# Performance work log

Measured on AMD Instinct MI355X. Metric: run time of the kernel, lower is better.

## Reference

```python
import jax, jax.numpy as jnp
import numpy as np

B, N, C = 2, 4096, 1024
H, WIN = 16, 20
D = C // H

def setup_inputs() -> dict:
    key = jax.random.key(0)
    ks = jax.random.split(key, 9)
    s = 1.0 / np.sqrt(C)
    d = {"q": jax.random.normal(ks[0], (B, N, C), jnp.float32)}
    for i, name in enumerate(["Wq", "Wk", "Wv", "Wo"]):
        d[name + "_w"] = jax.random.normal(ks[1 + 2 * i], (C, C), jnp.float32) * s
        d[name + "_b"] = jax.random.normal(ks[2 + 2 * i], (C,), jnp.float32) * 0.01
    return d

def reference(q, Wq_w, Wq_b, Wk_w, Wk_b, Wv_w, Wv_b, Wo_w, Wo_b):
    b, n, c = q.shape
    w2 = WIN // 2  # half window = 10
    def proj(x, w, bias):
        return (x @ w.T + bias).reshape(b, n, H, D).transpose(0, 2, 1, 3)  # [B,H,N,D]
    Q = proj(q, Wq_w, Wq_b)
    K = proj(q, Wk_w, Wk_b)
    V = proj(q, Wv_w, Wv_b)
    off = jnp.arange(-w2, w2 + 1)                       # [Wn] = 21 offsets
    pos = jnp.arange(n)[:, None] + off[None, :]         # [N, Wn] key index per query
    valid = (pos >= 0) & (pos < n)                      # edge clipping == torch start/end slicing
    idx = jnp.clip(pos, 0, n - 1)
    Kw = K[:, :, idx, :]                                # [B,H,N,Wn,D] gathered key windows
    Vw = V[:, :, idx, :]
    scale = jnp.sqrt(jnp.float32(D))
    scores = jnp.einsum('bhnd,bhnwd->bhnw', Q, Kw) / scale
    scores = jnp.where(valid[None, None], scores, -jnp.inf)
    probs = jax.nn.softmax(scores, axis=-1)             # invalid slots get exactly 0
    out = jnp.einsum('bhnw,bhnwd->bhnd', probs, Vw)
    out = out.transpose(0, 2, 1, 3).reshape(b, n, c)
    out = out @ Wo_w.T + Wo_b
    # torch returns attn_probs of the LAST loop iteration i=N-1: window [N-1-w2, N), size w2+1
    attn_last = probs[:, :, -1:, : w2 + 1]              # [B,H,1,11]
    return (out, attn_last)
```

## Files before the change

### kernel.cpp

```cpp
#include <hip/hip_runtime.h>
#include <hip/hip_bf16.h>

#define Bb 2
#define Nn 4096
#define Cc 1024
#define Hh 16
#define Dd 64
#define Mm (Bb*Nn)
#define W2 10
#define WINSZ 21

typedef __attribute__((ext_vector_type(8))) short  bf16x8s;
typedef __attribute__((ext_vector_type(4))) float  f32x4;
typedef __attribute__((ext_vector_type(4))) unsigned short us4;

#define AS1 __attribute__((address_space(1)))
#define AS3 __attribute__((address_space(3)))

__device__ __forceinline__ unsigned short f2bf(float f) {
  unsigned int u = __float_as_uint(f);
  u += 0x7FFFu + ((u >> 16) & 1u);
  return (unsigned short)(u >> 16);
}
__device__ __forceinline__ float bflo(unsigned int u) { return __uint_as_float(u << 16); }
__device__ __forceinline__ float bfhi(unsigned int u) { return __uint_as_float(u & 0xFFFF0000u); }

__global__ __launch_bounds__(256) void f2bf_kernel(const float4* __restrict__ src,
                                                   us4* __restrict__ dst, int n4) {
  int stride = gridDim.x * 256;
  for (int i = blockIdx.x * 256 + threadIdx.x; i < n4; i += stride) {
    float4 v = src[i];
    us4 o;
    o.x = f2bf(v.x); o.y = f2bf(v.y); o.z = f2bf(v.z); o.w = f2bf(v.w);
    dst[i] = o;
  }
}

template<bool OUT_BF16>
__global__ __launch_bounds__(512) void gemm_p3(const unsigned short* __restrict__ A,
                                               const unsigned short* __restrict__ Bm,
                                               const float* __restrict__ bias,
                                               void* __restrict__ Cout,
                                               int N) {
  constexpr int K = 1024, NT = 16;
  __shared__ unsigned short lds[3][24576];

  const int tid = threadIdx.x, wid = tid >> 6, lane = tid & 63;
  const int wm = wid >> 2, wn = wid & 3;

  const int nwg = gridDim.x, cpx = nwg >> 3, bid = blockIdx.x;
  const int swz = (bid & 7) * cpx + (bid >> 3);
  const int nbn = N >> 8;
  const int m0 = (swz / nbn) << 7, n0 = (swz % nbn) << 8;

  const int rbase = wid * 8 + (lane >> 3);
  const int cst = ((lane & 7) ^ (lane >> 3)) * 8;
  const unsigned short* aS0 = A + (size_t)(m0 + rbase) * K + cst;
  const unsigned short* aS1 = A + (size_t)(m0 + 64 + rbase) * K + cst;
  const unsigned short* bS0 = Bm + (size_t)(n0 + rbase) * K + cst;
  const unsigned short* bS1 = Bm + (size_t)(n0 + 64 + rbase) * K + cst;
  const unsigned short* bS2 = Bm + (size_t)(n0 + 128 + rbase) * K + cst;
  const unsigned short* bS3 = Bm + (size_t)(n0 + 192 + rbase) * K + cst;
  const int dA0 = wid * 512, dA1 = 4096 + wid * 512;
  const int dB0 = 8192 + wid * 512, dB1 = 12288 + wid * 512;
  const int dB2 = 16384 + wid * 512, dB3 = 20480 + wid * 512;

#define STG(bf, kt) do {                                                                   \
    const size_t ko = (size_t)(kt) * 64;                                                   \
    __builtin_amdgcn_global_load_lds((AS1 const void*)(aS0 + ko), (AS3 void*)(&lds[bf][dA0]), 16, 0, 0); \
    __builtin_amdgcn_global_load_lds((AS1 const void*)(aS1 + ko), (AS3 void*)(&lds[bf][dA1]), 16, 0, 0); \
    __builtin_amdgcn_global_load_lds((AS1 const void*)(bS0 + ko), (AS3 void*)(&lds[bf][dB0]), 16, 0, 0); \
    __builtin_amdgcn_global_load_lds((AS1 const void*)(bS1 + ko), (AS3 void*)(&lds[bf][dB1]), 16, 0, 0); \
    __builtin_amdgcn_global_load_lds((AS1 const void*)(bS2 + ko), (AS3 void*)(&lds[bf][dB2]), 16, 0, 0); \
    __builtin_amdgcn_global_load_lds((AS1 const void*)(bS3 + ko), (AS3 void*)(&lds[bf][dB3]), 16, 0, 0); \
  } while (0)

  int aoff[2][4], boff[2][4];
#pragma unroll
  for (int kk = 0; kk < 2; ++kk) {
    const int chs = ((kk * 4 + (lane >> 4)) ^ (lane & 7)) * 8;
#pragma unroll
    for (int f = 0; f < 4; ++f) {
      aoff[kk][f] = (wm * 64 + f * 16 + (lane & 15)) * 64 + chs;
      boff[kk][f] = 8192 + (wn * 64 + f * 16 + (lane & 15)) * 64 + chs;
    }
  }

  f32x4 acc[4][4] = {};

  STG(0, 0);
  STG(1, 1);
  asm volatile("s_waitcnt vmcnt(6)" ::: "memory");
  __builtin_amdgcn_sched_barrier(0);
  __builtin_amdgcn_s_barrier();
  __builtin_amdgcn_sched_barrier(0);

  int cur = 0, stg = 2;
  for (int t = 0; t < NT; ++t) {
    if (t + 2 < NT) STG(stg, t + 2);

    const unsigned short* L = &lds[cur][0];
    bf16x8s a[2][4], b[2][4];
#pragma unroll
    for (int kk = 0; kk < 2; ++kk) {
#pragma unroll
      for (int f = 0; f < 4; ++f) {
        a[kk][f] = *(const bf16x8s*)(L + aoff[kk][f]);
        b[kk][f] = *(const bf16x8s*)(L + boff[kk][f]);
      }
    }
    __builtin_amdgcn_s_setprio(1);
#pragma unroll
    for (int kk = 0; kk < 2; ++kk)
#pragma unroll
      for (int fm = 0; fm < 4; ++fm)
#pragma unroll
        for (int fn = 0; fn < 4; ++fn)
          acc[fm][fn] = __builtin_amdgcn_mfma_f32_16x16x32_bf16(a[kk][fm], b[kk][fn], acc[fm][fn], 0, 0, 0);
    __builtin_amdgcn_s_setprio(0);

    if (t + 1 < NT) {
      if (t + 2 < NT) asm volatile("s_waitcnt vmcnt(6)" ::: "memory");
      else            asm volatile("s_waitcnt vmcnt(0)" ::: "memory");
      __builtin_amdgcn_sched_barrier(0);
      __builtin_amdgcn_s_barrier();
      __builtin_amdgcn_sched_barrier(0);
    }
    cur = (cur == 2) ? 0 : cur + 1;
    stg = (stg == 2) ? 0 : stg + 1;
  }
#undef STG

  const int r0 = m0 + wm * 64 + (lane >> 4) * 4;
  const int c0 = n0 + wn * 64 + (lane & 15);
#pragma unroll
  for (int fm = 0; fm < 4; ++fm) {
#pragma unroll
    for (int fn = 0; fn < 4; ++fn) {
      const int col = c0 + fn * 16;
      const float bv = bias[col];
#pragma unroll
      for (int r = 0; r < 4; ++r) {
        const int row = r0 + fm * 16 + r;
        const float v = acc[fm][fn][r] + bv;
        if (OUT_BF16)
          ((unsigned short*)Cout)[(size_t)row * N + col] = f2bf(v);
        else
          ((float*)Cout)[(size_t)row * N + col] = v;
      }
    }
  }
}

#define TN 128
#define KVROWS (TN + 2 * W2)

__global__ void attn_kernel(const unsigned short* __restrict__ QKV,
                            unsigned short* __restrict__ AO,
                            float* __restrict__ attn_last) {
  __shared__ uint4 Kl[KVROWS * 8];
  __shared__ uint4 Vl[KVROWS * 8];

  const int nt = Nn / TN;
  const int bid = blockIdx.x;
  const int tile = bid & (nt - 1);
  const int bh = bid / nt;
  const int h = bh & (Hh - 1), b = bh / Hh;
  const int n0 = tile * TN;
  const int tid = threadIdx.x;

  for (int idx = tid; idx < KVROWS * 8; idx += 256) {
    const int r = idx >> 3, c = idx & 7;
    const int pos = n0 - W2 + r;
    uint4 kv = make_uint4(0, 0, 0, 0), vv = make_uint4(0, 0, 0, 0);
    if (pos >= 0 && pos < Nn) {
      const uint4* row = (const uint4*)(QKV + (size_t)(b * Nn + pos) * 3072);
      kv = row[128 + h * 8 + c];
      vv = row[256 + h * 8 + c];
    }
    const int slot = c ^ (r & 7);
    Kl[r * 8 + slot] = kv;
    Vl[r * 8 + slot] = vv;
  }
  __syncthreads();

  const int row  = tid >> 1;
  const int half = tid & 1;
  const int n = n0 + row;
  const size_t m = (size_t)b * Nn + n;

  const uint4* qrow = (const uint4*)(QKV + m * 3072) + h * 8 + half * 4;
  const uint4 qd0 = qrow[0], qd1 = qrow[1], qd2 = qrow[2], qd3 = qrow[3];

  float p[WINSZ];
#pragma unroll
  for (int w = 0; w < WINSZ; ++w) p[w] = 0.f;

#pragma unroll
  for (int c = 0; c < 4; ++c) {
    const uint4 qv = (c == 0) ? qd0 : (c == 1) ? qd1 : (c == 2) ? qd2 : qd3;
    const float q0 = bflo(qv.x), q1 = bfhi(qv.x);
    const float q2 = bflo(qv.y), q3 = bfhi(qv.y);
    const float q4 = bflo(qv.z), q5 = bfhi(qv.z);
    const float q6 = bflo(qv.w), q7 = bfhi(qv.w);
#pragma unroll 7
    for (int w = 0; w < WINSZ; ++w) {
      const int r = row + w;
      const uint4 v = Kl[r * 8 + ((half * 4 + c) ^ (r & 7))];
      float a0 = q0 * bflo(v.x);
      float a1 = q1 * bfhi(v.x);
      a0 += q2 * bflo(v.y);
      a1 += q3 * bfhi(v.y);
      a0 += q4 * bflo(v.z);
      a1 += q5 * bfhi(v.z);
      a0 += q6 * bflo(v.w);
      a1 += q7 * bfhi(v.w);
      p[w] += a0 + a1;
    }
  }

#pragma unroll
  for (int w = 0; w < WINSZ; ++w) {
    float t = p[w];
    t += __shfl_xor(t, 1, 64);
    const int pos = n - W2 + w;
    p[w] = (pos < 0 || pos >= Nn) ? -1e30f : t * 0.125f;
  }
  float mx = p[0];
#pragma unroll
  for (int w = 1; w < WINSZ; ++w) mx = fmaxf(mx, p[w]);
  float sum = 0.f;
#pragma unroll
  for (int w = 0; w < WINSZ; ++w) { p[w] = __expf(p[w] - mx); sum += p[w]; }
  const float inv = 1.0f / sum;

  if (n == Nn - 1 && half == 0) {
#pragma unroll
    for (int w = 0; w <= W2; ++w)
      attn_last[(b * Hh + h) * (W2 + 1) + w] = p[w] * inv;
  }

  uint4* orow = (uint4*)(AO + m * Cc + h * Dd) + half * 4;
#pragma unroll
  for (int c = 0; c < 4; ++c) {
    float o0 = 0.f, o1 = 0.f, o2 = 0.f, o3 = 0.f;
    float o4 = 0.f, o5 = 0.f, o6 = 0.f, o7 = 0.f;
#pragma unroll 7
    for (int w = 0; w < WINSZ; ++w) {
      const int r = row + w;
      const uint4 v = Vl[r * 8 + ((half * 4 + c) ^ (r & 7))];
      const float pw = p[w];
      o0 += pw * bflo(v.x);
      o1 += pw * bfhi(v.x);
      o2 += pw * bflo(v.y);
      o3 += pw * bfhi(v.y);
      o4 += pw * bflo(v.z);
      o5 += pw * bfhi(v.z);
      o6 += pw * bflo(v.w);
      o7 += pw * bfhi(v.w);
    }
    unsigned int d0 = (unsigned int)f2bf(o0 * inv) | ((unsigned int)f2bf(o1 * inv) << 16);
    unsigned int d1 = (unsigned int)f2bf(o2 * inv) | ((unsigned int)f2bf(o3 * inv) << 16);
    unsigned int d2 = (unsigned int)f2bf(o4 * inv) | ((unsigned int)f2bf(o5 * inv) << 16);
    unsigned int d3 = (unsigned int)f2bf(o6 * inv) | ((unsigned int)f2bf(o7 * inv) << 16);
    orow[c] = make_uint4(d0, d1, d2, d3);
  }
}

extern "C" void kernel_launch(void* const* d_in, const int* in_sizes, int n_in,
                              void* d_out, int out_size, void* d_ws, size_t ws_size,
                              hipStream_t stream) {
  const float* q    = (const float*)d_in[0];
  const float* Wq_w = (const float*)d_in[1];
  const float* Wq_b = (const float*)d_in[2];
  const float* Wk_w = (const float*)d_in[3];
  const float* Wk_b = (const float*)d_in[4];
  const float* Wv_w = (const float*)d_in[5];
  const float* Wv_b = (const float*)d_in[6];
  const float* Wo_w = (const float*)d_in[7];
  const float* Wo_b = (const float*)d_in[8];
  float* out = (float*)d_out;
  float* attn_last = out + (size_t)Mm * Cc;

  char* ws = (char*)d_ws;
  unsigned short* qb   = (unsigned short*)(ws);
  unsigned short* Wqkv = (unsigned short*)(ws + 16777216);
  unsigned short* Wo16 = (unsigned short*)(ws + 16777216 + 6291456);
  float*          bqkv = (float*)(ws + 25165824);
  unsigned short* QKV  = (unsigned short*)(ws + 25182208);
  unsigned short* AO   = (unsigned short*)(ws + 75513856);

  {
    int n4 = (Mm * Cc) / 4;
    f2bf_kernel<<<2048, 256, 0, stream>>>((const float4*)q, (us4*)qb, n4);
    int w4 = (Cc * Cc) / 4;
    f2bf_kernel<<<1024, 256, 0, stream>>>((const float4*)Wq_w, (us4*)(Wqkv), w4);
    f2bf_kernel<<<1024, 256, 0, stream>>>((const float4*)Wk_w, (us4*)(Wqkv + Cc * Cc), w4);
    f2bf_kernel<<<1024, 256, 0, stream>>>((const float4*)Wv_w, (us4*)(Wqkv + 2 * Cc * Cc), w4);
    f2bf_kernel<<<1024, 256, 0, stream>>>((const float4*)Wo_w, (us4*)Wo16, w4);
    hipMemcpyAsync(bqkv,          Wq_b, Cc * sizeof(float), hipMemcpyDeviceToDevice, stream);
    hipMemcpyAsync(bqkv + Cc,     Wk_b, Cc * sizeof(float), hipMemcpyDeviceToDevice, stream);
    hipMemcpyAsync(bqkv + 2 * Cc, Wv_b, Cc * sizeof(float), hipMemcpyDeviceToDevice, stream);
  }

  {
    dim3 grid((Mm / 128) * (3072 / 256));
    gemm_p3<true><<<grid, 512, 0, stream>>>(qb, Wqkv, bqkv, (void*)QKV, 3072);
  }

  {
    dim3 grid(Bb * Hh * (Nn / TN));
    attn_kernel<<<grid, 256, 0, stream>>>(QKV, AO, attn_last);
  }

  {
    dim3 grid((Mm / 128) * (Cc / 256));
    gemm_p3<false><<<grid, 512, 0, stream>>>(AO, Wo16, Wo_b, (void*)out, Cc);
  }
}
```

Baseline: 150.7 us.

## Fuse conversion kernels into one launch and switch GEMM to K=32 tiles

Five separate fp32-to-bf16 conversion launches and three bias memcpys are merged into a single grid-stride kernel, which removes launch and memcpy overhead. Separately, the GEMM k-tile shrinks from 64 to 32. That halves LDS use per stage, drops the XOR swizzle, and doubles the number of main-loop iterations and barriers. The unswizzled LDS layout may cause bank conflicts, and the extra barriers add synchronization cost.

New measurement: 145.9 us. -3.2%, faster.

```diff
diff --git a/kernel.cpp b/kernel.cpp
--- a/kernel.cpp
+++ b/kernel.cpp
@@ -25,25 +25,53 @@
 __device__ __forceinline__ float bflo(unsigned int u) { return __uint_as_float(u << 16); }
 __device__ __forceinline__ float bfhi(unsigned int u) { return __uint_as_float(u & 0xFFFF0000u); }
 
-__global__ __launch_bounds__(256) void f2bf_kernel(const float4* __restrict__ src,
-                                                   us4* __restrict__ dst, int n4) {
-  int stride = gridDim.x * 256;
-  for (int i = blockIdx.x * 256 + threadIdx.x; i < n4; i += stride) {
-    float4 v = src[i];
-    us4 o;
-    o.x = f2bf(v.x); o.y = f2bf(v.y); o.z = f2bf(v.z); o.w = f2bf(v.w);
-    dst[i] = o;
+__device__ __forceinline__ us4 cvt4(float4 v) {
+  us4 o;
+  o.x = f2bf(v.x); o.y = f2bf(v.y); o.z = f2bf(v.z); o.w = f2bf(v.w);
+  return o;
+}
+
+__global__ __launch_bounds__(256) void cvt_all(const float4* __restrict__ q,
+                                               const float4* __restrict__ wq,
+                                               const float4* __restrict__ wk,
+                                               const float4* __restrict__ wv,
+                                               const float4* __restrict__ wo,
+                                               const float* __restrict__ bq,
+                                               const float* __restrict__ bk,
+                                               const float* __restrict__ bv,
+                                               us4* __restrict__ qb4,
+                                               us4* __restrict__ wqkv4,
+                                               us4* __restrict__ wo4,
+                                               float* __restrict__ bqkv) {
+  const int NQ = 2097152, NW = 262144, TOT = NQ + 4 * NW;
+  const int gid = blockIdx.x * 256 + threadIdx.x;
+  const int stride = gridDim.x * 256;
+  for (int i = gid; i < TOT; i += stride) {
+    if (i < NQ) {
+      qb4[i] = cvt4(q[i]);
+    } else {
+      int j = i - NQ;
+      int r = j >> 18, k = j & (NW - 1);
+      if (r == 0)      wqkv4[k]          = cvt4(wq[k]);
+      else if (r == 1) wqkv4[NW + k]     = cvt4(wk[k]);
+      else if (r == 2) wqkv4[2 * NW + k] = cvt4(wv[k]);
+      else             wo4[k]            = cvt4(wo[k]);
+    }
+  }
+  if (gid < 3072) {
+    float v = (gid < 1024) ? bq[gid] : (gid < 2048) ? bk[gid - 1024] : bv[gid - 2048];
+    bqkv[gid] = v;
   }
 }
 
 template<bool OUT_BF16>
-__global__ __launch_bounds__(512) void gemm_p3(const unsigned short* __restrict__ A,
-                                               const unsigned short* __restrict__ Bm,
-                                               const float* __restrict__ bias,
-                                               void* __restrict__ Cout,
-                                               int N) {
-  constexpr int K = 1024, NT = 16;
-  __shared__ unsigned short lds[3][24576];
+__global__ __launch_bounds__(512) void gemm_k32(const unsigned short* __restrict__ A,
+                                                const unsigned short* __restrict__ Bm,
+                                                const float* __restrict__ bias,
+                                                void* __restrict__ Cout,
+                                                int N) {
+  constexpr int K = 1024, NT = 32;
+  __shared__ unsigned short lds[3][12288];
 
   const int tid = threadIdx.x, wid = tid >> 6, lane = tid & 63;
   const int wm = wid >> 2, wn = wid & 3;
@@ -53,81 +81,60 @@
   const int nbn = N >> 8;
   const int m0 = (swz / nbn) << 7, n0 = (swz % nbn) << 8;
 
-  const int rbase = wid * 8 + (lane >> 3);
-  const int cst = ((lane & 7) ^ (lane >> 3)) * 8;
-  const unsigned short* aS0 = A + (size_t)(m0 + rbase) * K + cst;
-  const unsigned short* aS1 = A + (size_t)(m0 + 64 + rbase) * K + cst;
-  const unsigned short* bS0 = Bm + (size_t)(n0 + rbase) * K + cst;
-  const unsigned short* bS1 = Bm + (size_t)(n0 + 64 + rbase) * K + cst;
-  const unsigned short* bS2 = Bm + (size_t)(n0 + 128 + rbase) * K + cst;
-  const unsigned short* bS3 = Bm + (size_t)(n0 + 192 + rbase) * K + cst;
-  const int dA0 = wid * 512, dA1 = 4096 + wid * 512;
-  const int dB0 = 8192 + wid * 512, dB1 = 12288 + wid * 512;
-  const int dB2 = 16384 + wid * 512, dB3 = 20480 + wid * 512;
-
-#define STG(bf, kt) do {                                                                   \
-    const size_t ko = (size_t)(kt) * 64;                                                   \
-    __builtin_amdgcn_global_load_lds((AS1 const void*)(aS0 + ko), (AS3 void*)(&lds[bf][dA0]), 16, 0, 0); \
-    __builtin_amdgcn_global_load_lds((AS1 const void*)(aS1 + ko), (AS3 void*)(&lds[bf][dA1]), 16, 0, 0); \
+  const unsigned short* aS  = A  + (size_t)(m0 + wid * 16 + (lane >> 2)) * K + (lane & 3) * 8;
+  const unsigned short* bS0 = Bm + (size_t)(n0 + wid * 32 + (lane >> 2)) * K + (lane & 3) * 8;
+  const unsigned short* bS1 = bS0 + (size_t)16 * K;
+  const int dA = wid * 512, dB0 = 4096 + wid * 1024, dB1 = 4096 + wid * 1024 + 512;
+
+#define STG(bf, kt) do {                                                                      \
+    const size_t ko = (size_t)(kt) * 32;                                                      \
+    __builtin_amdgcn_global_load_lds((AS1 const void*)(aS  + ko), (AS3 void*)(&lds[bf][dA ]), 16, 0, 0); \
     __builtin_amdgcn_global_load_lds((AS1 const void*)(bS0 + ko), (AS3 void*)(&lds[bf][dB0]), 16, 0, 0); \
     __builtin_amdgcn_global_load_lds((AS1 const void*)(bS1 + ko), (AS3 void*)(&lds[bf][dB1]), 16, 0, 0); \
-    __builtin_amdgcn_global_load_lds((AS1 const void*)(bS2 + ko), (AS3 void*)(&lds[bf][dB2]), 16, 0, 0); \
-    __builtin_amdgcn_global_load_lds((AS1 const void*)(bS3 + ko), (AS3 void*)(&lds[bf][dB3]), 16, 0, 0); \
   } while (0)
 
-  int aoff[2][4], boff[2][4];
-#pragma unroll
-  for (int kk = 0; kk < 2; ++kk) {
-    const int chs = ((kk * 4 + (lane >> 4)) ^ (lane & 7)) * 8;
-#pragma unroll
-    for (int f = 0; f < 4; ++f) {
-      aoff[kk][f] = (wm * 64 + f * 16 + (lane & 15)) * 64 + chs;
-      boff[kk][f] = 8192 + (wn * 64 + f * 16 + (lane & 15)) * 64 + chs;
-    }
+  int aoff[4], boff[4];
+#pragma unroll
+  for (int f = 0; f < 4; ++f) {
+    aoff[f] = (wm * 64 + f * 16 + (lane & 15)) * 32 + (lane >> 4) * 8;
+    boff[f] = 4096 + (wn * 64 + f * 16 + (lane & 15)) * 32 + (lane >> 4) * 8;
   }
 
   f32x4 acc[4][4] = {};
 
   STG(0, 0);
   STG(1, 1);
-  asm volatile("s_waitcnt vmcnt(6)" ::: "memory");
+  asm volatile("s_waitcnt vmcnt(3)" ::: "memory");
   __builtin_amdgcn_sched_barrier(0);
   __builtin_amdgcn_s_barrier();
   __builtin_amdgcn_sched_barrier(0);
 
-  int cur = 0, stg = 2;
+#pragma unroll 4
   for (int t = 0; t < NT; ++t) {
-    if (t + 2 < NT) STG(stg, t + 2);
+    const int cur = t % 3;
+    if (t + 2 < NT) STG((t + 2) % 3, t + 2);
 
     const unsigned short* L = &lds[cur][0];
-    bf16x8s a[2][4], b[2][4];
-#pragma unroll
-    for (int kk = 0; kk < 2; ++kk) {
-#pragma unroll
-      for (int f = 0; f < 4; ++f) {
-        a[kk][f] = *(const bf16x8s*)(L + aoff[kk][f]);
-        b[kk][f] = *(const bf16x8s*)(L + boff[kk][f]);
-      }
-    }
+    bf16x8s a[4], b[4];
+#pragma unroll
+    for (int f = 0; f < 4; ++f) a[f] = *(const bf16x8s*)(L + aoff[f]);
+#pragma unroll
+    for (int f = 0; f < 4; ++f) b[f] = *(const bf16x8s*)(L + boff[f]);
     __builtin_amdgcn_s_setprio(1);
 #pragma unroll
-    for (int kk = 0; kk < 2; ++kk)
-#pragma unroll
-      for (int fm = 0; fm < 4; ++fm)
-#pragma unroll
-        for (int fn = 0; fn < 4; ++fn)
-          acc[fm][fn] = __builtin_amdgcn_mfma_f32_16x16x32_bf16(a[kk][fm], b[kk][fn], acc[fm][fn], 0, 0, 0);
+    for (int fm = 0; fm < 4; ++fm)
+#pragma unroll
+      for (int fn = 0; fn < 4; ++fn)
+        acc[fm][fn] = __builtin_amdgcn_mfma_f32_16x16x32_bf16(a[fm], b[fn], acc[fm][fn], 0, 0, 0);
     __builtin_amdgcn_s_setprio(0);
 
     if (t + 1 < NT) {
-      if (t + 2 < NT) asm volatile("s_waitcnt vmcnt(6)" ::: "memory");
+      if (t + 2 < NT) asm volatile("s_waitcnt vmcnt(3)" ::: "memory");
       else            asm volatile("s_waitcnt vmcnt(0)" ::: "memory");
       __builtin_amdgcn_sched_barrier(0);
       __builtin_amdgcn_s_barrier();
       __builtin_amdgcn_sched_barrier(0);
     }
-    cur = (cur == 2) ? 0 : cur + 1;
-    stg = (stg == 2) ? 0 : stg + 1;
   }
 #undef STG
 
@@ -290,22 +297,15 @@
   unsigned short* QKV  = (unsigned short*)(ws + 25182208);
   unsigned short* AO   = (unsigned short*)(ws + 75513856);
 
-  {
-    int n4 = (Mm * Cc) / 4;
-    f2bf_kernel<<<2048, 256, 0, stream>>>((const float4*)q, (us4*)qb, n4);
-    int w4 = (Cc * Cc) / 4;
-    f2bf_kernel<<<1024, 256, 0, stream>>>((const float4*)Wq_w, (us4*)(Wqkv), w4);
-    f2bf_kernel<<<1024, 256, 0, stream>>>((const float4*)Wk_w, (us4*)(Wqkv + Cc * Cc), w4);
-    f2bf_kernel<<<1024, 256, 0, stream>>>((const float4*)Wv_w, (us4*)(Wqkv + 2 * Cc * Cc), w4);
-    f2bf_kernel<<<1024, 256, 0, stream>>>((const float4*)Wo_w, (us4*)Wo16, w4);
-    hipMemcpyAsync(bqkv,          Wq_b, Cc * sizeof(float), hipMemcpyDeviceToDevice, stream);
-    hipMemcpyAsync(bqkv + Cc,     Wk_b, Cc * sizeof(float), hipMemcpyDeviceToDevice, stream);
-    hipMemcpyAsync(bqkv + 2 * Cc, Wv_b, Cc * sizeof(float), hipMemcpyDeviceToDevice, stream);
-  }
+  cvt_all<<<2048, 256, 0, stream>>>((const float4*)q,
+                                    (const float4*)Wq_w, (const float4*)Wk_w,
+                                    (const float4*)Wv_w, (const float4*)Wo_w,
+                                    Wq_b, Wk_b, Wv_b,
+                                    (us4*)qb, (us4*)Wqkv, (us4*)Wo16, bqkv);
 
   {
     dim3 grid((Mm / 128) * (3072 / 256));
-    gemm_p3<true><<<grid, 512, 0, stream>>>(qb, Wqkv, bqkv, (void*)QKV, 3072);
+    gemm_k32<true><<<grid, 512, 0, stream>>>(qb, Wqkv, bqkv, (void*)QKV, 3072);
   }
 
   {
@@ -315,6 +315,6 @@
 
   {
     dim3 grid((Mm / 128) * (Cc / 256));
-    gemm_p3<false><<<grid, 512, 0, stream>>>(AO, Wo16, Wo_b, (void*)out, Cc);
-  }
-}
+    gemm_k32<false><<<grid, 512, 0, stream>>>(AO, Wo16, Wo_b, (void*)out, Cc);
+  }
+}
```
